# Performance work log

Measured on AMD Instinct MI355X. Metric: run time of the kernel, lower is better.

The kernel has to match this reference:

```python
import jax, jax.numpy as jnp
import numpy as np

B, T, D, H = 4, 2048, 1024, 16
HD = D // H  # head dim = 64


def setup_inputs() -> dict:
    key = jax.random.key(0)
    ks = jax.random.split(key, 6)
    s = 0.02
    return {
        "x": jax.random.normal(ks[0], (B, T, D), dtype=jnp.float32),
        "Wk": jax.random.normal(ks[1], (D, D), dtype=jnp.float32) * s,
        "Wq": jax.random.normal(ks[2], (D, D), dtype=jnp.float32) * s,
        "Wv": jax.random.normal(ks[3], (D, D), dtype=jnp.float32) * s,
        "Wp": jax.random.normal(ks[4], (D, D), dtype=jnp.float32) * s,
        "bp": jnp.zeros((D,), dtype=jnp.float32),
    }


def reference(x, Wk, Wq, Wv, Wp, bp):
    # nn.Linear applies x @ W.T; weights here are stored torch-style [out, in]
    Bq, Tq, _ = x.shape
    k = (x @ Wk.T).reshape(Bq, Tq, H, HD).transpose(0, 2, 1, 3)  # [B,H,T,hd]
    q = (x @ Wq.T).reshape(Bq, Tq, H, HD).transpose(0, 2, 1, 3)
    v = (x @ Wv.T).reshape(Bq, Tq, H, HD).transpose(0, 2, 1, 3)
    scale = HD ** -0.5
    attn = jnp.einsum('bhqd,bhkd->bhqk', q, k) * scale  # [B,H,T,T]
    causal = jnp.tril(jnp.ones((Tq, Tq), dtype=bool))
    attn = jnp.where(causal, attn, -jnp.inf)
    attn = jax.nn.softmax(attn, axis=-1)
    # dropout p=0.0 -> identity (eval semantics)
    out = jnp.einsum('bhqk,bhkd->bhqd', attn, v)  # [B,H,T,hd]
    out = out.transpose(0, 2, 1, 3).reshape(Bq, Tq, D)
    return out @ Wp.T + bp
```

## Files before the change

### kernel.cpp

```cpp
#include <hip/hip_runtime.h>
#include <hip/hip_bf16.h>
#include <stdint.h>


typedef __bf16 bf16x8 __attribute__((ext_vector_type(8)));
typedef float floatx4 __attribute__((ext_vector_type(4)));
typedef unsigned short ushort_t;
typedef unsigned short ushortx8 __attribute__((ext_vector_type(8)));
typedef unsigned short ushortx4 __attribute__((ext_vector_type(4)));

#define MFMA16(a, b, c) __builtin_amdgcn_mfma_f32_16x16x32_bf16((a), (b), (c), 0, 0, 0)

static __device__ __forceinline__ ushort_t f2bfu(float f) {
  union { float f; unsigned u; } v; v.f = f;
  unsigned r = v.u + 0x7FFFu + ((v.u >> 16) & 1u);
  return (ushort_t)(r >> 16);
}
static __device__ __forceinline__ ushort_t f2bfu_trunc(float f) {
  union { float f; unsigned u; } v; v.f = f;
  return (ushort_t)(v.u >> 16);
}

static __device__ __forceinline__ void gl_lds16(const void* g, void* l) {
  __builtin_amdgcn_global_load_lds(
      (const __attribute__((address_space(1))) void*)g,
      (__attribute__((address_space(3))) void*)l, 16, 0, 0);
}

__global__ void cvt_all(const float* __restrict__ x,  const float* __restrict__ wk,
                        const float* __restrict__ wq, const float* __restrict__ wv,
                        const float* __restrict__ wp, ushortx4* __restrict__ dst) {
  const int i = blockIdx.x * blockDim.x + threadIdx.x;
  const float4* src; int off;
  if (i < 2097152) { src = (const float4*)x; off = i; }
  else {
    const int r = i - 2097152;
    const int sel = r >> 18;
    off = r & 262143;
    src = (const float4*)(sel == 0 ? wk : sel == 1 ? wq : sel == 2 ? wv : wp);
  }
  const float4 f = src[off];
  ushortx4 o;
  o[0] = f2bfu(f.x); o[1] = f2bfu(f.y); o[2] = f2bfu(f.z); o[3] = f2bfu(f.w);
  dst[i] = o;
}

__global__ __launch_bounds__(256) void gemm_qkv(
    const ushort_t* __restrict__ X,
    const ushort_t* __restrict__ Wq, const ushort_t* __restrict__ Wk,
    const ushort_t* __restrict__ Wv,
    ushort_t* __restrict__ qtb, ushort_t* __restrict__ kb, ushort_t* __restrict__ vtb)
{
  const int z = blockIdx.z;
  const ushort_t* Bm = (z == 0) ? Wq : (z == 1) ? Wk : Wv;
  __shared__ ushort_t Al[128 * 64];
  __shared__ ushort_t Bl[128 * 64];
  const int tid = threadIdx.x;
  const int w = tid >> 6, lane = tid & 63, g = lane >> 4, c = lane & 15;
  const int wm = w >> 1, wn = w & 1;
  const int cswz = c & 7;
  const int m0 = blockIdx.x * 128, n0 = blockIdx.y * 128;

  floatx4 acc[4][4];
  const floatx4 zero4 = {0.f, 0.f, 0.f, 0.f};
#pragma unroll
  for (int i = 0; i < 4; ++i)
#pragma unroll
    for (int j = 0; j < 4; ++j) acc[i][j] = zero4;

  const int srow = tid >> 3;
  const int gsw  = ((tid & 7) ^ (srow & 7)) * 8;

  for (int k0 = 0; k0 < 1024; k0 += 64) {
#pragma unroll
    for (int p = 0; p < 4; ++p) {
      const int row = p * 32 + srow;
      gl_lds16(&X [(size_t)(m0 + row) * 1024 + k0 + gsw], &Al[p * 2048 + tid * 8]);
      gl_lds16(&Bm[(size_t)(n0 + row) * 1024 + k0 + gsw], &Bl[p * 2048 + tid * 8]);
    }
    __syncthreads();
#pragma unroll
    for (int kk = 0; kk < 2; ++kk) {
      bf16x8 af[4], bfr[4];
#pragma unroll
      for (int i = 0; i < 4; ++i) {
        const int sw = ((kk * 4 + g) ^ cswz) * 8;
        af[i]  = *reinterpret_cast<const bf16x8*>(&Al[(wm * 64 + i * 16 + c) * 64 + sw]);
        bfr[i] = *reinterpret_cast<const bf16x8*>(&Bl[(wn * 64 + i * 16 + c) * 64 + sw]);
      }
#pragma unroll
      for (int i = 0; i < 4; ++i)
#pragma unroll
        for (int j = 0; j < 4; ++j)
          acc[i][j] = MFMA16(af[i], bfr[j], acc[i][j]);
    }
    __syncthreads();
  }

#pragma unroll
  for (int i = 0; i < 4; ++i) {
#pragma unroll
    for (int j = 0; j < 4; ++j) {
      const int mbase = m0 + wm * 64 + i * 16 + g * 4;
      const int n = n0 + wn * 64 + j * 16 + c;
      const int h = n >> 6, d = n & 63;
      if (z != 1) {
        ushort_t* ob = (z == 0) ? qtb : vtb;
        const int bb = mbase >> 11, t = mbase & 2047;
        ushortx4 pk;
#pragma unroll
        for (int r = 0; r < 4; ++r) pk[r] = f2bfu(acc[i][j][r]);
        *reinterpret_cast<ushortx4*>(&ob[(size_t)((bb * 16 + h) * 64 + d) * 2048 + t]) = pk;
      } else {
#pragma unroll
        for (int r = 0; r < 4; ++r) {
          const int m = mbase + r;
          const int bb = m >> 11, t = m & 2047;
          kb[(size_t)((bb * 16 + h) * 2048 + t) * 64 + d] = f2bfu(acc[i][j][r]);
        }
      }
    }
  }
}

__global__ __launch_bounds__(256) void attn_kernel(
    const ushort_t* __restrict__ qtbuf, const ushort_t* __restrict__ kbuf,
    const ushort_t* __restrict__ vtbuf, ushort_t* __restrict__ obuf)
{
  const int j = blockIdx.x, h = blockIdx.y, b = blockIdx.z;
  const int tid = threadIdx.x, w = tid >> 6, lane = tid & 63, g = lane >> 4, c = lane & 15;

  __shared__ ushort_t Kl[128 * 64];
  __shared__ ushort_t Vl[64 * 128];
  __shared__ ushort_t Pl[4][16 * 72];

  const size_t bh = (size_t)(b * 16 + h);
  const ushort_t* kb_bh = kbuf + bh * 2048 * 64;
  const ushort_t* vt_bh = vtbuf + bh * 64 * 2048;
  const ushort_t* qt_bh = qtbuf + bh * 64 * 2048;

  const int rb0 = j * 64 + w * 16;
  const int rb1 = (31 - j) * 64 + w * 16;

  bf16x8 aq0[2], aq1[2];
  {
    union { ushortx8 u; bf16x8 v; } t00, t01, t10, t11;
#pragma unroll
    for (int jj = 0; jj < 8; ++jj) {
      const int d0 = g * 8 + jj, d1 = 32 + g * 8 + jj;
      t00.u[jj] = qt_bh[(size_t)d0 * 2048 + rb0 + c];
      t01.u[jj] = qt_bh[(size_t)d1 * 2048 + rb0 + c];
      t10.u[jj] = qt_bh[(size_t)d0 * 2048 + rb1 + c];
      t11.u[jj] = qt_bh[(size_t)d1 * 2048 + rb1 + c];
    }
    aq0[0] = t00.v; aq0[1] = t01.v; aq1[0] = t10.v; aq1[1] = t11.v;
  }

  floatx4 oacc0[4], oacc1[4];
  float lp0[4], lp1[4];
  const floatx4 zero4 = {0.f, 0.f, 0.f, 0.f};
#pragma unroll
  for (int td = 0; td < 4; ++td) { oacc0[td] = zero4; oacc1[td] = zero4; }
#pragma unroll
  for (int r = 0; r < 4; ++r) { lp0[r] = 0.f; lp1[r] = 0.f; }

  const int krow_s = tid >> 3;
  const int kgsw   = ((tid & 7) ^ (krow_s & 7)) * 8;
  const int vrow_s = tid >> 4;
  const int vgsw   = ((tid & 15) ^ (vrow_s & 15)) * 8;

  const int n128 = (33 - j) >> 1;
  for (int kt = 0; kt < n128; ++kt) {
    const int key0 = kt * 128;
#pragma unroll
    for (int p = 0; p < 4; ++p) {
      const int kr = p * 32 + krow_s;
      gl_lds16(&kb_bh[(size_t)(key0 + kr) * 64 + kgsw], &Kl[p * 2048 + tid * 8]);
      const int vr = p * 16 + vrow_s;
      gl_lds16(&vt_bh[(size_t)vr * 2048 + key0 + vgsw], &Vl[p * 2048 + tid * 8]);
    }
    __syncthreads();

#pragma unroll
    for (int s = 0; s < 2; ++s) {
      const int ti = 2 * kt + s;
      const int key0s = ti * 64;
#pragma unroll
      for (int grp = 0; grp < 2; ++grp) {
        const int lim = (grp == 0) ? j : 31 - j;
        if (ti > lim) continue;
        const int rb = (grp == 0) ? rb0 : rb1;
        const bf16x8 a0 = (grp == 0) ? aq0[0] : aq1[0];
        const bf16x8 a1 = (grp == 0) ? aq0[1] : aq1[1];

        float pv[4][4];
#pragma unroll
        for (int t4 = 0; t4 < 4; ++t4) {
          const int krow = s * 64 + t4 * 16 + c;
          const bf16x8 k0f = *reinterpret_cast<const bf16x8*>(&Kl[krow * 64 + ((g) ^ (c & 7)) * 8]);
          const bf16x8 k1f = *reinterpret_cast<const bf16x8*>(&Kl[krow * 64 + ((4 + g) ^ (c & 7)) * 8]);
          floatx4 sa = zero4;
          sa = MFMA16(a0, k0f, sa);
          sa = MFMA16(a1, k1f, sa);
          if (ti == lim) {
            const int key = key0s + t4 * 16 + c;
#pragma unroll
            for (int r = 0; r < 4; ++r) {
              const float e = __expf(sa[r] * 0.125f);
              pv[t4][r] = (key <= rb + g * 4 + r) ? e : 0.f;
            }
          } else {
#pragma unroll
            for (int r = 0; r < 4; ++r) pv[t4][r] = __expf(sa[r] * 0.125f);
          }
        }
#pragma unroll
        for (int r = 0; r < 4; ++r) {
          const float sm = (pv[0][r] + pv[1][r]) + (pv[2][r] + pv[3][r]);
          if (grp == 0) lp0[r] += sm; else lp1[r] += sm;
        }

        ushort_t* pw = Pl[w];
#pragma unroll
        for (int t4 = 0; t4 < 4; ++t4)
#pragma unroll
          for (int r = 0; r < 4; ++r)
            pw[(g * 4 + r) * 72 + t4 * 16 + c] = f2bfu_trunc(pv[t4][r]);
        const bf16x8 ap0 = *reinterpret_cast<const bf16x8*>(&pw[c * 72 + g * 8]);
        const bf16x8 ap1 = *reinterpret_cast<const bf16x8*>(&pw[c * 72 + 32 + g * 8]);
#pragma unroll
        for (int td = 0; td < 4; ++td) {
          const int vrow = td * 16 + c;
          const bf16x8 bv0 = *reinterpret_cast<const bf16x8*>(&Vl[vrow * 128 + ((s * 8 + g) ^ c) * 8]);
          const bf16x8 bv1 = *reinterpret_cast<const bf16x8*>(&Vl[vrow * 128 + ((s * 8 + 4 + g) ^ c) * 8]);
          if (grp == 0) {
            oacc0[td] = MFMA16(ap0, bv0, oacc0[td]);
            oacc0[td] = MFMA16(ap1, bv1, oacc0[td]);
          } else {
            oacc1[td] = MFMA16(ap0, bv0, oacc1[td]);
            oacc1[td] = MFMA16(ap1, bv1, oacc1[td]);
          }
        }
      }
    }
    __syncthreads();
  }

#pragma unroll
  for (int grp = 0; grp < 2; ++grp) {
    const int rb = (grp == 0) ? rb0 : rb1;
#pragma unroll
    for (int r = 0; r < 4; ++r) {
      float ls = (grp == 0) ? lp0[r] : lp1[r];
#pragma unroll
      for (int o = 1; o < 16; o <<= 1) ls += __shfl_xor(ls, o, 64);
      const float inv = 1.f / ls;
      const int q = rb + g * 4 + r;
#pragma unroll
      for (int td = 0; td < 4; ++td) {
        const int d = td * 16 + c;
        const float ov = ((grp == 0) ? oacc0[td][r] : oacc1[td][r]) * inv;
        obuf[((size_t)(b * 2048 + q) * 16 + h) * 64 + d] = f2bfu(ov);
      }
    }
  }
}

__global__ __launch_bounds__(256) void gemm_proj(
    const ushort_t* __restrict__ A, const ushort_t* __restrict__ Wp,
    const float* __restrict__ bias, float* __restrict__ out)
{
  __shared__ ushort_t Al[128 * 64];
  __shared__ ushort_t Bl[128 * 64];
  const int tid = threadIdx.x;
  const int w = tid >> 6, lane = tid & 63, g = lane >> 4, c = lane & 15;
  const int wm = w >> 1, wn = w & 1;
  const int cswz = c & 7;
  const int m0 = blockIdx.x * 128, n0 = blockIdx.y * 128;

  floatx4 acc[4][4];
  const floatx4 zero4 = {0.f, 0.f, 0.f, 0.f};
#pragma unroll
  for (int i = 0; i < 4; ++i)
#pragma unroll
    for (int j = 0; j < 4; ++j) acc[i][j] = zero4;

  const int srow = tid >> 3;
  const int gsw  = ((tid & 7) ^ (srow & 7)) * 8;

  for (int k0 = 0; k0 < 1024; k0 += 64) {
#pragma unroll
    for (int p = 0; p < 4; ++p) {
      const int row = p * 32 + srow;
      gl_lds16(&A [(size_t)(m0 + row) * 1024 + k0 + gsw], &Al[p * 2048 + tid * 8]);
      gl_lds16(&Wp[(size_t)(n0 + row) * 1024 + k0 + gsw], &Bl[p * 2048 + tid * 8]);
    }
    __syncthreads();
#pragma unroll
    for (int kk = 0; kk < 2; ++kk) {
      bf16x8 af[4], bfr[4];
#pragma unroll
      for (int i = 0; i < 4; ++i) {
        const int sw = ((kk * 4 + g) ^ cswz) * 8;
        af[i]  = *reinterpret_cast<const bf16x8*>(&Al[(wm * 64 + i * 16 + c) * 64 + sw]);
        bfr[i] = *reinterpret_cast<const bf16x8*>(&Bl[(wn * 64 + i * 16 + c) * 64 + sw]);
      }
#pragma unroll
      for (int i = 0; i < 4; ++i)
#pragma unroll
        for (int j = 0; j < 4; ++j)
          acc[i][j] = MFMA16(af[i], bfr[j], acc[i][j]);
    }
    __syncthreads();
  }

#pragma unroll
  for (int i = 0; i < 4; ++i) {
#pragma unroll
    for (int j = 0; j < 4; ++j) {
      const int n = n0 + wn * 64 + j * 16 + c;
      const float bv = bias[n];
#pragma unroll
      for (int r = 0; r < 4; ++r) {
        const int m = m0 + wm * 64 + i * 16 + g * 4 + r;
        out[(size_t)m * 1024 + n] = acc[i][j][r] + bv;
      }
    }
  }
}

extern "C" void kernel_launch(void* const* d_in, const int* in_sizes, int n_in,
                              void* d_out, int out_size, void* d_ws, size_t ws_size,
                              hipStream_t stream) {
  const float* x  = (const float*)d_in[0];
  const float* Wk = (const float*)d_in[1];
  const float* Wq = (const float*)d_in[2];
  const float* Wv = (const float*)d_in[3];
  const float* Wp = (const float*)d_in[4];
  const float* bp = (const float*)d_in[5];
  float* out = (float*)d_out;

  char* ws = (char*)d_ws;
  const size_t SZ_X = (size_t)8192 * 1024 * 2;
  const size_t SZ_W = (size_t)1024 * 1024 * 2;
  ushort_t* xb    = (ushort_t*)ws;  ws += SZ_X;
  ushort_t* wkb   = (ushort_t*)ws;  ws += SZ_W;
  ushort_t* wqb   = (ushort_t*)ws;  ws += SZ_W;
  ushort_t* wvb   = (ushort_t*)ws;  ws += SZ_W;
  ushort_t* wpb   = (ushort_t*)ws;  ws += SZ_W;
  ushort_t* qtbuf = (ushort_t*)ws;  ws += SZ_X;
  ushort_t* kbuf  = (ushort_t*)ws;  ws += SZ_X;
  ushort_t* vtbuf = (ushort_t*)ws;  ws += SZ_X;
  ushort_t* obuf  = xb;

  cvt_all<<<12288, 256, 0, stream>>>(x, Wk, Wq, Wv, Wp, (ushortx4*)xb);

  gemm_qkv<<<dim3(64, 8, 3), 256, 0, stream>>>(xb, wqb, wkb, wvb, qtbuf, kbuf, vtbuf);
  attn_kernel<<<dim3(16, 16, 4), 256, 0, stream>>>(qtbuf, kbuf, vtbuf, obuf);
  gemm_proj<<<dim3(64, 8), 256, 0, stream>>>(obuf, wpb, bp, out);
}
```

Measured before the change: 266.9 us.

## Compute transposed scores so P stays in registers for PV MFMA

```diff
diff --git a/kernel.cpp b/kernel.cpp
--- a/kernel.cpp
+++ b/kernel.cpp
@@ -8,17 +8,20 @@
 typedef unsigned short ushort_t;
 typedef unsigned short ushortx8 __attribute__((ext_vector_type(8)));
 typedef unsigned short ushortx4 __attribute__((ext_vector_type(4)));
+typedef short shortx4 __attribute__((ext_vector_type(4)));
 
 #define MFMA16(a, b, c) __builtin_amdgcn_mfma_f32_16x16x32_bf16((a), (b), (c), 0, 0, 0)
+#define MFMA16K16(a, b, c) __builtin_amdgcn_mfma_f32_16x16x16bf16_1k((a), (b), (c), 0, 0, 0)
+#define EXP2F(x) __builtin_amdgcn_exp2f(x)
 
 static __device__ __forceinline__ ushort_t f2bfu(float f) {
   union { float f; unsigned u; } v; v.f = f;
   unsigned r = v.u + 0x7FFFu + ((v.u >> 16) & 1u);
   return (ushort_t)(r >> 16);
 }
-static __device__ __forceinline__ ushort_t f2bfu_trunc(float f) {
-  union { float f; unsigned u; } v; v.f = f;
-  return (ushort_t)(v.u >> 16);
+
+static __device__ __forceinline__ unsigned pack_bf2(float lo, float hi) {
+  return __builtin_amdgcn_perm(__float_as_uint(hi), __float_as_uint(lo), 0x07060302);
 }
 
 static __device__ __forceinline__ void gl_lds16(const void* g, void* l) {
@@ -49,7 +52,7 @@
     const ushort_t* __restrict__ X,
     const ushort_t* __restrict__ Wq, const ushort_t* __restrict__ Wk,
     const ushort_t* __restrict__ Wv,
-    ushort_t* __restrict__ qtb, ushort_t* __restrict__ kb, ushort_t* __restrict__ vtb)
+    ushort_t* __restrict__ qb, ushort_t* __restrict__ kb, ushort_t* __restrict__ vtb)
 {
   const int z = blockIdx.z;
   const ushort_t* Bm = (z == 0) ? Wq : (z == 1) ? Wk : Wv;
@@ -104,27 +107,27 @@
       const int mbase = m0 + wm * 64 + i * 16 + g * 4;
       const int n = n0 + wn * 64 + j * 16 + c;
       const int h = n >> 6, d = n & 63;
-      if (z != 1) {
-        ushort_t* ob = (z == 0) ? qtb : vtb;
+      if (z == 2) {
         const int bb = mbase >> 11, t = mbase & 2047;
         ushortx4 pk;
 #pragma unroll
         for (int r = 0; r < 4; ++r) pk[r] = f2bfu(acc[i][j][r]);
-        *reinterpret_cast<ushortx4*>(&ob[(size_t)((bb * 16 + h) * 64 + d) * 2048 + t]) = pk;
+        *reinterpret_cast<ushortx4*>(&vtb[(size_t)((bb * 16 + h) * 64 + d) * 2048 + t]) = pk;
       } else {
+        ushort_t* ob = (z == 0) ? qb : kb;
 #pragma unroll
         for (int r = 0; r < 4; ++r) {
           const int m = mbase + r;
           const int bb = m >> 11, t = m & 2047;
-          kb[(size_t)((bb * 16 + h) * 2048 + t) * 64 + d] = f2bfu(acc[i][j][r]);
+          ob[(size_t)((bb * 16 + h) * 2048 + t) * 64 + d] = f2bfu(acc[i][j][r]);
         }
       }
     }
   }
 }
 
-__global__ __launch_bounds__(256) void attn_kernel(
-    const ushort_t* __restrict__ qtbuf, const ushort_t* __restrict__ kbuf,
+__global__ __launch_bounds__(256, 4) void attn_kernel(
+    const ushort_t* __restrict__ qbuf, const ushort_t* __restrict__ kbuf,
     const ushort_t* __restrict__ vtbuf, ushort_t* __restrict__ obuf)
 {
   const int j = blockIdx.x, h = blockIdx.y, b = blockIdx.z;
@@ -132,42 +135,37 @@
 
   __shared__ ushort_t Kl[128 * 64];
   __shared__ ushort_t Vl[64 * 128];
-  __shared__ ushort_t Pl[4][16 * 72];
 
   const size_t bh = (size_t)(b * 16 + h);
   const ushort_t* kb_bh = kbuf + bh * 2048 * 64;
   const ushort_t* vt_bh = vtbuf + bh * 64 * 2048;
-  const ushort_t* qt_bh = qtbuf + bh * 64 * 2048;
+  const ushort_t* qb_bh = qbuf + bh * 2048 * 64;
 
   const int rb0 = j * 64 + w * 16;
   const int rb1 = (31 - j) * 64 + w * 16;
 
   bf16x8 aq0[2], aq1[2];
   {
-    union { ushortx8 u; bf16x8 v; } t00, t01, t10, t11;
-#pragma unroll
-    for (int jj = 0; jj < 8; ++jj) {
-      const int d0 = g * 8 + jj, d1 = 32 + g * 8 + jj;
-      t00.u[jj] = qt_bh[(size_t)d0 * 2048 + rb0 + c];
-      t01.u[jj] = qt_bh[(size_t)d1 * 2048 + rb0 + c];
-      t10.u[jj] = qt_bh[(size_t)d0 * 2048 + rb1 + c];
-      t11.u[jj] = qt_bh[(size_t)d1 * 2048 + rb1 + c];
-    }
-    aq0[0] = t00.v; aq0[1] = t01.v; aq1[0] = t10.v; aq1[1] = t11.v;
+    const ushort_t* qp0 = qb_bh + (size_t)(rb0 + c) * 64;
+    aq0[0] = *reinterpret_cast<const bf16x8*>(qp0 + g * 8);
+    aq0[1] = *reinterpret_cast<const bf16x8*>(qp0 + 32 + g * 8);
+    const ushort_t* qp1 = qb_bh + (size_t)(rb1 + c) * 64;
+    aq1[0] = *reinterpret_cast<const bf16x8*>(qp1 + g * 8);
+    aq1[1] = *reinterpret_cast<const bf16x8*>(qp1 + 32 + g * 8);
   }
 
   floatx4 oacc0[4], oacc1[4];
-  float lp0[4], lp1[4];
+  float l0 = 0.f, l1 = 0.f;
   const floatx4 zero4 = {0.f, 0.f, 0.f, 0.f};
 #pragma unroll
   for (int td = 0; td < 4; ++td) { oacc0[td] = zero4; oacc1[td] = zero4; }
-#pragma unroll
-  for (int r = 0; r < 4; ++r) { lp0[r] = 0.f; lp1[r] = 0.f; }
 
   const int krow_s = tid >> 3;
   const int kgsw   = ((tid & 7) ^ (krow_s & 7)) * 8;
   const int vrow_s = tid >> 4;
   const int vgsw   = ((tid & 15) ^ (vrow_s & 15)) * 8;
+
+  const float SCALE = 0.18033688011112042f;
 
   const int n128 = (33 - j) >> 1;
   for (int kt = 0; kt < n128; ++kt) {
@@ -190,8 +188,8 @@
         const int lim = (grp == 0) ? j : 31 - j;
         if (ti > lim) continue;
         const int rb = (grp == 0) ? rb0 : rb1;
-        const bf16x8 a0 = (grp == 0) ? aq0[0] : aq1[0];
-        const bf16x8 a1 = (grp == 0) ? aq0[1] : aq1[1];
+        const bf16x8 b0 = (grp == 0) ? aq0[0] : aq1[0];
+        const bf16x8 b1 = (grp == 0) ? aq0[1] : aq1[1];
 
         float pv[4][4];
 #pragma unroll
@@ -200,45 +198,40 @@
           const bf16x8 k0f = *reinterpret_cast<const bf16x8*>(&Kl[krow * 64 + ((g) ^ (c & 7)) * 8]);
           const bf16x8 k1f = *reinterpret_cast<const bf16x8*>(&Kl[krow * 64 + ((4 + g) ^ (c & 7)) * 8]);
           floatx4 sa = zero4;
-          sa = MFMA16(a0, k0f, sa);
-          sa = MFMA16(a1, k1f, sa);
+          sa = MFMA16(k0f, b0, sa);
+          sa = MFMA16(k1f, b1, sa);
           if (ti == lim) {
-            const int key = key0s + t4 * 16 + c;
+            const int q = rb + c;
 #pragma unroll
             for (int r = 0; r < 4; ++r) {
-              const float e = __expf(sa[r] * 0.125f);
-              pv[t4][r] = (key <= rb + g * 4 + r) ? e : 0.f;
+              const int key = key0s + t4 * 16 + g * 4 + r;
+              const float e = EXP2F(sa[r] * SCALE);
+              pv[t4][r] = (key <= q) ? e : 0.f;
             }
           } else {
 #pragma unroll
-            for (int r = 0; r < 4; ++r) pv[t4][r] = __expf(sa[r] * 0.125f);
+            for (int r = 0; r < 4; ++r) pv[t4][r] = EXP2F(sa[r] * SCALE);
           }
         }
-#pragma unroll
-        for (int r = 0; r < 4; ++r) {
-          const float sm = (pv[0][r] + pv[1][r]) + (pv[2][r] + pv[3][r]);
-          if (grp == 0) lp0[r] += sm; else lp1[r] += sm;
-        }
-
-        ushort_t* pw = Pl[w];
+        float lsum = 0.f;
 #pragma unroll
         for (int t4 = 0; t4 < 4; ++t4)
-#pragma unroll
-          for (int r = 0; r < 4; ++r)
-            pw[(g * 4 + r) * 72 + t4 * 16 + c] = f2bfu_trunc(pv[t4][r]);
-        const bf16x8 ap0 = *reinterpret_cast<const bf16x8*>(&pw[c * 72 + g * 8]);
-        const bf16x8 ap1 = *reinterpret_cast<const bf16x8*>(&pw[c * 72 + 32 + g * 8]);
-#pragma unroll
-        for (int td = 0; td < 4; ++td) {
-          const int vrow = td * 16 + c;
-          const bf16x8 bv0 = *reinterpret_cast<const bf16x8*>(&Vl[vrow * 128 + ((s * 8 + g) ^ c) * 8]);
-          const bf16x8 bv1 = *reinterpret_cast<const bf16x8*>(&Vl[vrow * 128 + ((s * 8 + 4 + g) ^ c) * 8]);
-          if (grp == 0) {
-            oacc0[td] = MFMA16(ap0, bv0, oacc0[td]);
-            oacc0[td] = MFMA16(ap1, bv1, oacc0[td]);
-          } else {
-            oacc1[td] = MFMA16(ap0, bv0, oacc1[td]);
-            oacc1[td] = MFMA16(ap1, bv1, oacc1[td]);
+          lsum += (pv[t4][0] + pv[t4][1]) + (pv[t4][2] + pv[t4][3]);
+        if (grp == 0) l0 += lsum; else l1 += lsum;
+
+#pragma unroll
+        for (int t4 = 0; t4 < 4; ++t4) {
+          union { unsigned u[2]; shortx4 v; } pk;
+          pk.u[0] = pack_bf2(pv[t4][0], pv[t4][1]);
+          pk.u[1] = pack_bf2(pv[t4][2], pv[t4][3]);
+          const int cc = s * 8 + t4 * 2 + (g >> 1);
+          const int ko = (g & 1) * 4;
+#pragma unroll
+          for (int td = 0; td < 4; ++td) {
+            const shortx4 va = *reinterpret_cast<const shortx4*>(
+                &Vl[(td * 16 + c) * 128 + (cc ^ c) * 8 + ko]);
+            if (grp == 0) oacc0[td] = MFMA16K16(va, pk.v, oacc0[td]);
+            else          oacc1[td] = MFMA16K16(va, pk.v, oacc1[td]);
           }
         }
       }
@@ -248,20 +241,19 @@
 
 #pragma unroll
   for (int grp = 0; grp < 2; ++grp) {
-    const int rb = (grp == 0) ? rb0 : rb1;
-#pragma unroll
-    for (int r = 0; r < 4; ++r) {
-      float ls = (grp == 0) ? lp0[r] : lp1[r];
-#pragma unroll
-      for (int o = 1; o < 16; o <<= 1) ls += __shfl_xor(ls, o, 64);
-      const float inv = 1.f / ls;
-      const int q = rb + g * 4 + r;
-#pragma unroll
-      for (int td = 0; td < 4; ++td) {
-        const int d = td * 16 + c;
-        const float ov = ((grp == 0) ? oacc0[td][r] : oacc1[td][r]) * inv;
-        obuf[((size_t)(b * 2048 + q) * 16 + h) * 64 + d] = f2bfu(ov);
-      }
+    float ls = (grp == 0) ? l0 : l1;
+    ls += __shfl_xor(ls, 16, 64);
+    ls += __shfl_xor(ls, 32, 64);
+    const float inv = 1.f / ls;
+    const int q = ((grp == 0) ? rb0 : rb1) + c;
+    ushort_t* ob = &obuf[((size_t)(b * 2048 + q) * 16 + h) * 64];
+#pragma unroll
+    for (int td = 0; td < 4; ++td) {
+      const floatx4 oa = (grp == 0) ? oacc0[td] : oacc1[td];
+      ushortx4 pk;
+#pragma unroll
+      for (int r = 0; r < 4; ++r) pk[r] = f2bfu(oa[r] * inv);
+      *reinterpret_cast<ushortx4*>(&ob[td * 16 + g * 4]) = pk;
     }
   }
 }
@@ -348,14 +340,14 @@
   ushort_t* wqb   = (ushort_t*)ws;  ws += SZ_W;
   ushort_t* wvb   = (ushort_t*)ws;  ws += SZ_W;
   ushort_t* wpb   = (ushort_t*)ws;  ws += SZ_W;
-  ushort_t* qtbuf = (ushort_t*)ws;  ws += SZ_X;
+  ushort_t* qbuf  = (ushort_t*)ws;  ws += SZ_X;
   ushort_t* kbuf  = (ushort_t*)ws;  ws += SZ_X;
   ushort_t* vtbuf = (ushort_t*)ws;  ws += SZ_X;
   ushort_t* obuf  = xb;
 
   cvt_all<<<12288, 256, 0, stream>>>(x, Wk, Wq, Wv, Wp, (ushortx4*)xb);
 
-  gemm_qkv<<<dim3(64, 8, 3), 256, 0, stream>>>(xb, wqb, wkb, wvb, qtbuf, kbuf, vtbuf);
-  attn_kernel<<<dim3(16, 16, 4), 256, 0, stream>>>(qtbuf, kbuf, vtbuf, obuf);
+  gemm_qkv<<<dim3(64, 8, 3), 256, 0, stream>>>(xb, wqb, wkb, wvb, qbuf, kbuf, vtbuf);
+  attn_kernel<<<dim3(16, 16, 4), 256, 0, stream>>>(qbuf, kbuf, vtbuf, obuf);
   gemm_proj<<<dim3(64, 8), 256, 0, stream>>>(obuf, wpb, bp, out);
 }
```

Result: faster. 251.4 us (-5.8%).
